# Kernel optimization log

Measured on AMD Instinct MI355X. Metric: run time of the kernel, lower is better.

## Reference

```python
import jax, jax.numpy as jnp
import numpy as np

EMBED_DIM = 512
KDIM = 64
VDIM = 64


def setup_inputs() -> dict:
    key = jax.random.key(0)
    kx, kq, kk, kv = jax.random.split(key, 4)
    B, S = 4, 4096
    x = jax.random.normal(kx, (B, S, EMBED_DIM), dtype=jnp.float32)
    # nn.Linear(embed_dim, out) weight has shape [out, embed_dim]
    WQ = jax.random.normal(kq, (KDIM, EMBED_DIM), dtype=jnp.float32) * (EMBED_DIM ** -0.5)
    WK = jax.random.normal(kk, (KDIM, EMBED_DIM), dtype=jnp.float32) * (EMBED_DIM ** -0.5)
    WV = jax.random.normal(kv, (VDIM, EMBED_DIM), dtype=jnp.float32) * (EMBED_DIM ** -0.5)
    return {"x": x, "WQ": WQ, "WK": WK, "WV": WV}


def reference(x, WQ, WK, WV):
    # q,k: [B,S,kdim]; v: [B,S,vdim] (self-attention: x[0] is x[-1])
    q = jnp.einsum('bse,ke->bsk', x, WQ)
    k = jnp.einsum('bse,ke->bsk', x, WK)
    v = jnp.einsum('bse,ve->bsv', x, WV)
    scale = k.shape[-1] ** -0.5
    scores = jnp.einsum('bqk,bsk->bqs', q, k) * scale  # [B,S,S]
    # dropout p=0.0 -> identity; masked branch in source is a no-op (non-in-place masked_fill discarded)
    attn = jax.nn.softmax(scores, axis=-1)
    out = jnp.einsum('bqs,bsv->bqv', attn, v)  # [B,S,vdim]
    return out
```

## Files before the change

### kernel.cpp

```cpp
#include <hip/hip_runtime.h>

#define BATCH 4
#define SEQ   4096
#define EMB   512
#define HD    64

typedef __attribute__((ext_vector_type(8))) short short8;
typedef __attribute__((ext_vector_type(4))) float floatx4;

static __device__ __forceinline__ unsigned short f2bf(float f) {
  unsigned u = __builtin_bit_cast(unsigned, f);
  u += 0x7fffu + ((u >> 16) & 1u);
  return (unsigned short)(u >> 16);
}
static __device__ __forceinline__ float bf2f(unsigned short h) {
  unsigned u = ((unsigned)h) << 16;
  return __builtin_bit_cast(float, u);
}
static __device__ __forceinline__ unsigned pack_hi16(float lo, float hi) {
#if __has_builtin(__builtin_amdgcn_perm)
  return __builtin_amdgcn_perm(__builtin_bit_cast(unsigned, hi),
                               __builtin_bit_cast(unsigned, lo), 0x07060302u);
#else
  return (__builtin_bit_cast(unsigned, lo) >> 16) |
         (__builtin_bit_cast(unsigned, hi) & 0xffff0000u);
#endif
}
static __device__ __forceinline__ unsigned pack_f16(float a, float b) {
#if __has_builtin(__builtin_amdgcn_cvt_pkrtz)
  typedef __fp16 fp16v2 __attribute__((ext_vector_type(2)));
  fp16v2 h = __builtin_amdgcn_cvt_pkrtz(a, b);
  return __builtin_bit_cast(unsigned, h);
#else
  _Float16 ha = (_Float16)a, hb = (_Float16)b;
  return (unsigned)__builtin_bit_cast(unsigned short, ha) |
         ((unsigned)__builtin_bit_cast(unsigned short, hb) << 16);
#endif
}
static __device__ __forceinline__ float f16_to_f32(unsigned short bits) {
  _Float16 h = __builtin_bit_cast(_Float16, bits);
  return (float)h;
}

__global__ __launch_bounds__(256) void convw_kernel(
    const float* __restrict__ WQ, const float* __restrict__ WK,
    const float* __restrict__ WV, unsigned short* __restrict__ Wpk)
{
  int t = blockIdx.x * 256 + threadIdx.x;
  int p    = t >> 12;
  int w    = (t >> 10) & 3;
  int kc   = (t >> 6) & 15;
  int lane = t & 63;
  int lr = lane & 15, g = lane >> 4;
  const float* src = (p == 0) ? WQ : ((p == 1) ? WK : WV);
  const float4* s4 = (const float4*)(src + (16 * w + lr) * EMB + kc * 32 + 8 * g);
  float4 a = s4[0], b = s4[1];
  float vv[8] = {a.x, a.y, a.z, a.w, b.x, b.y, b.z, b.w};
  short8 o;
#pragma unroll
  for (int j = 0; j < 8; ++j) {
    unsigned short h = f2bf(vv[j]);
    o[j] = (p == 3) ? (short)f2bf(vv[j] - bf2f(h)) : (short)h;
  }
  *(short8*)(Wpk + (size_t)t * 8) = o;
}

#define XST 40

__global__ __launch_bounds__(256) void proj_kernel(
    const float* __restrict__ x,
    const unsigned short* __restrict__ Wpk,
    unsigned short* __restrict__ Qb,
    unsigned short* __restrict__ Kb,
    unsigned short* __restrict__ VTb)
{
  __shared__ __align__(16) unsigned short Xh[2][32 * XST];
  __shared__ __align__(16) unsigned short Xl[2][32 * XST];

  const int tid  = threadIdx.x;
  const int lane = tid & 63;
  const int w    = tid >> 6;
  const int lr   = lane & 15, g = lane >> 4;
  const long rowBase = (long)blockIdx.x * 32;

  floatx4 accQ[2], accK[2], accV[2];
#pragma unroll
  for (int rt = 0; rt < 2; ++rt) {
    floatx4 z = {0.f, 0.f, 0.f, 0.f};
    accQ[rt] = z; accK[rt] = z; accV[rt] = z;
  }

  const int srow = tid >> 3;
  const int sc   = 4 * (tid & 7);
  const float* xbase = x + (rowBase + srow) * EMB + sc;

  auto stage_write = [&](float4 v, int buf) {
    float vv[4] = {v.x, v.y, v.z, v.w};
    ushort4 hi, lo;
#pragma unroll
    for (int i = 0; i < 4; ++i) {
      unsigned short h = f2bf(vv[i]);
      ((unsigned short*)&hi)[i] = h;
      ((unsigned short*)&lo)[i] = f2bf(vv[i] - bf2f(h));
    }
    *(ushort4*)&Xh[buf][srow * XST + sc] = hi;
    *(ushort4*)&Xl[buf][srow * XST + sc] = lo;
  };

  float4 xv = *(const float4*)(xbase);
  stage_write(xv, 0);
  float4 xnxt = *(const float4*)(xbase + 32);

#pragma unroll 2
  for (int kc = 0; kc < 16; ++kc) {
    __syncthreads();
    const unsigned short* wb = Wpk + (size_t)(w * 16 + kc) * 512 + lane * 8;
    short8 wq  = *(const short8*)(wb);
    short8 wk  = *(const short8*)(wb + 32768);
    short8 wvh = *(const short8*)(wb + 2 * 32768);
    short8 wvl = *(const short8*)(wb + 3 * 32768);
    float4 xfut;
    if (kc + 2 < 16) xfut = *(const float4*)(xbase + (kc + 2) * 32);
    const int buf = kc & 1;
#pragma unroll
    for (int rt = 0; rt < 2; ++rt) {
      short8 xh = *(const short8*)&Xh[buf][(16 * rt + lr) * XST + 8 * g];
      short8 xl = *(const short8*)&Xl[buf][(16 * rt + lr) * XST + 8 * g];
      accQ[rt] = __builtin_amdgcn_mfma_f32_16x16x32_bf16(wq, xh, accQ[rt], 0, 0, 0);
      accK[rt] = __builtin_amdgcn_mfma_f32_16x16x32_bf16(wk, xh, accK[rt], 0, 0, 0);
      accV[rt] = __builtin_amdgcn_mfma_f32_16x16x32_bf16(xh, wvh, accV[rt], 0, 0, 0);
      accV[rt] = __builtin_amdgcn_mfma_f32_16x16x32_bf16(xl, wvh, accV[rt], 0, 0, 0);
      accV[rt] = __builtin_amdgcn_mfma_f32_16x16x32_bf16(xh, wvl, accV[rt], 0, 0, 0);
    }
    if (kc + 1 < 16) { stage_write(xnxt, (kc + 1) & 1); xnxt = xfut; }
  }

  const int bb  = (int)(rowBase >> 12);
  const int sIn = (int)(rowBase & 4095);
#pragma unroll
  for (int rt = 0; rt < 2; ++rt) {
    {
      long row = rowBase + 16 * rt + lr;
      int  col = 16 * w + 4 * g;
      ushort4 u; u.x = f2bf(accQ[rt][0]); u.y = f2bf(accQ[rt][1]);
      u.z = f2bf(accQ[rt][2]); u.w = f2bf(accQ[rt][3]);
      *(ushort4*)(Qb + row * HD + col) = u;
      ushort4 v; v.x = f2bf(accK[rt][0]); v.y = f2bf(accK[rt][1]);
      v.z = f2bf(accK[rt][2]); v.w = f2bf(accK[rt][3]);
      *(ushort4*)(Kb + row * HD + col) = v;
    }
    {
      long addr = ((long)(bb * 64 + 16 * w + lr)) * SEQ + sIn + 16 * rt + 4 * g;
      ushort4 u; u.x = f2bf(accV[rt][0]); u.y = f2bf(accV[rt][1]);
      u.z = f2bf(accV[rt][2]); u.w = f2bf(accV[rt][3]);
      *(ushort4*)(VTb + addr) = u;
    }
  }
}

#define PST 72

__global__ __launch_bounds__(256, 2) void flash_kernel(
    const unsigned short* __restrict__ Qb,
    const unsigned short* __restrict__ Kb,
    const unsigned short* __restrict__ VTb,
    unsigned short* __restrict__ Opart,
    float* __restrict__ Lpart)
{
  __shared__ __align__(16) unsigned short K0lds[64 * 64];
  __shared__ __align__(16) unsigned short V0lds[64 * 64];
  __shared__ __align__(16) unsigned short K1lds[64 * 64];
  __shared__ __align__(16) unsigned short V1lds[64 * 64];
  __shared__ __align__(16) unsigned short Plds[4][64 * PST];

  const int tid  = threadIdx.x;
  const int lane = tid & 63;
  const int w    = tid >> 6;
  const int lr   = lane & 15, g = lane >> 4;
  const int qb   = blockIdx.x >> 3;
  const int ks   = blockIdx.x & 7;
  const int bb   = qb >> 4;
  const long qrow0 = (long)qb * 256 + 64 * w;
  const int  kbase = ks * 512;

  short8 qf[4][2];
#pragma unroll
  for (int qh = 0; qh < 4; ++qh)
#pragma unroll
    for (int ec = 0; ec < 2; ++ec)
      qf[qh][ec] = *(const short8*)(Qb + (qrow0 + 16 * qh + lr) * HD + ec * 32 + 8 * g);

  floatx4 accO[4][4];
#pragma unroll
  for (int qh = 0; qh < 4; ++qh)
#pragma unroll
    for (int t = 0; t < 4; ++t) { floatx4 z = {0.f,0.f,0.f,0.f}; accO[qh][t] = z; }
  float lsum[4] = {0.f, 0.f, 0.f, 0.f};
  const float cp = 0.18033688011112042f;
  const float SH = 2.0f;

#define STAGE(kt_, KL, VL) do {                                               \
    const int k0_ = kbase + (kt_) * 64;                                       \
    _Pragma("unroll")                                                         \
    for (int h_ = 0; h_ < 2; ++h_) {                                          \
      int ci_  = h_ * 256 + tid;                                              \
      int row_ = ci_ >> 3;                                                    \
      int cc_  = (ci_ & 7) ^ (row_ & 7);                                      \
      const unsigned short* gK_ = Kb + ((long)bb * SEQ + k0_ + row_) * HD + cc_ * 8; \
      __builtin_amdgcn_global_load_lds(                                       \
          (const __attribute__((address_space(1))) void*)gK_,                 \
          (__attribute__((address_space(3))) void*)((KL) + ci_ * 8), 16, 0, 0); \
      const unsigned short* gV_ = VTb + ((long)bb * HD + row_) * SEQ + k0_ + cc_ * 8; \
      __builtin_amdgcn_global_load_lds(                                       \
          (const __attribute__((address_space(1))) void*)gV_,                 \
          (__attribute__((address_space(3))) void*)((VL) + ci_ * 8), 16, 0, 0); \
    }                                                                         \
  } while (0)

#define COMPUTE(KL, VL) do {                                                  \
    short8 kf[2][4];                                                          \
    _Pragma("unroll")                                                         \
    for (int ec = 0; ec < 2; ++ec)                                            \
      _Pragma("unroll")                                                       \
      for (int t = 0; t < 4; ++t) {                                           \
        int key  = 16 * t + lr;                                               \
        int slot = key * 8 + ((4 * ec + g) ^ (key & 7));                      \
        kf[ec][t] = *(const short8*)((KL) + slot * 8);                        \
      }                                                                       \
    _Pragma("unroll")                                                         \
    for (int qh = 0; qh < 4; ++qh) {                                          \
      floatx4 s_[4];                                                          \
      _Pragma("unroll")                                                       \
      for (int t = 0; t < 4; ++t) { floatx4 z = {0.f,0.f,0.f,0.f}; s_[t] = z; } \
      _Pragma("unroll")                                                       \
      for (int ec = 0; ec < 2; ++ec)                                          \
        _Pragma("unroll")                                                     \
        for (int t = 0; t < 4; ++t)                                           \
          s_[t] = __builtin_amdgcn_mfma_f32_16x16x32_bf16(kf[ec][t], qf[qh][ec], s_[t], 0, 0, 0); \
      unsigned short* prow = &Plds[w][(16 * qh + lr) * PST];                  \
      float ls = 0.0f;                                                        \
      _Pragma("unroll")                                                       \
      for (int t = 0; t < 4; ++t) {                                           \
        float p0 = __builtin_amdgcn_exp2f(__builtin_fmaf(s_[t][0], cp, -SH)); \
        float p1 = __builtin_amdgcn_exp2f(__builtin_fmaf(s_[t][1], cp, -SH)); \
        float p2 = __builtin_amdgcn_exp2f(__builtin_fmaf(s_[t][2], cp, -SH)); \
        float p3 = __builtin_amdgcn_exp2f(__builtin_fmaf(s_[t][3], cp, -SH)); \
        uint2 u;                                                              \
        u.x = pack_hi16(p0, p1);                                              \
        u.y = pack_hi16(p2, p3);                                              \
        ls += __builtin_bit_cast(float, u.x << 16);                           \
        ls += __builtin_bit_cast(float, u.x & 0xffff0000u);                   \
        ls += __builtin_bit_cast(float, u.y << 16);                           \
        ls += __builtin_bit_cast(float, u.y & 0xffff0000u);                   \
        *(uint2*)(prow + 16 * t + 4 * g) = u;                                 \
      }                                                                       \
      lsum[qh] += ls;                                                         \
    }                                                                         \
    short8 vf[2][4];                                                          \
    _Pragma("unroll")                                                         \
    for (int c = 0; c < 2; ++c)                                               \
      _Pragma("unroll")                                                       \
      for (int t = 0; t < 4; ++t) {                                           \
        int d    = 16 * t + lr;                                               \
        int slot = d * 8 + ((4 * c + g) ^ (d & 7));                           \
        vf[c][t] = *(const short8*)((VL) + slot * 8);                         \
      }                                                                       \
    _Pragma("unroll")                                                         \
    for (int qh = 0; qh < 4; ++qh)                                            \
      _Pragma("unroll")                                                       \
      for (int c = 0; c < 2; ++c) {                                           \
        short8 pf = *(const short8*)(&Plds[w][(16 * qh + lr) * PST + 32 * c + 8 * g]); \
        _Pragma("unroll")                                                     \
        for (int t = 0; t < 4; ++t)                                           \
          accO[qh][t] = __builtin_amdgcn_mfma_f32_16x16x32_bf16(vf[c][t], pf, accO[qh][t], 0, 0, 0); \
      }                                                                       \
  } while (0)

  STAGE(0, K0lds, V0lds);
  for (int kt = 0; kt < 8; kt += 2) {
    __syncthreads();
    STAGE(kt + 1, K1lds, V1lds);
    COMPUTE(K0lds, V0lds);
    __syncthreads();
    if (kt + 2 < 8) STAGE(kt + 2, K0lds, V0lds);
    COMPUTE(K1lds, V1lds);
  }
#undef STAGE
#undef COMPUTE

  unsigned short* obase = Opart + (size_t)(qb * 8 + ks) * 256 * HD;
#pragma unroll
  for (int qh = 0; qh < 4; ++qh) {
    float l = lsum[qh];
    l += __shfl_xor(l, 16, 64);
    l += __shfl_xor(l, 32, 64);
    int qlocal = 64 * w + 16 * qh + lr;
#pragma unroll
    for (int t = 0; t < 4; ++t) {
      uint2 u;
      u.x = pack_f16(accO[qh][t][0], accO[qh][t][1]);
      u.y = pack_f16(accO[qh][t][2], accO[qh][t][3]);
      *(uint2*)(obase + qlocal * HD + 16 * t + 4 * g) = u;
    }
    if (g == 0) Lpart[(qb * 8 + ks) * 256 + qlocal] = l;
  }
}

__global__ __launch_bounds__(256) void combine_kernel(
    const unsigned short* __restrict__ Opart, const float* __restrict__ Lpart,
    float* __restrict__ out)
{
  int t   = blockIdx.x * 256 + threadIdx.x;
  int row = t >> 4;
  int d0  = (t & 15) * 4;
  int qb = row >> 8, qi = row & 255;
  float4 acc = {0.f, 0.f, 0.f, 0.f};
  float lt = 0.0f;
#pragma unroll
  for (int ks = 0; ks < 8; ++ks) {
    const unsigned short* p = Opart + ((size_t)(qb * 8 + ks) * 256 + qi) * HD + d0;
    ushort4 v = *(const ushort4*)p;
    acc.x += f16_to_f32(v.x);
    acc.y += f16_to_f32(v.y);
    acc.z += f16_to_f32(v.z);
    acc.w += f16_to_f32(v.w);
    lt += Lpart[(qb * 8 + ks) * 256 + qi];
  }
  float inv = 1.0f / lt;
  float4 o = {acc.x * inv, acc.y * inv, acc.z * inv, acc.w * inv};
  *(float4*)(out + (size_t)row * HD + d0) = o;
}

extern "C" void kernel_launch(void* const* d_in, const int* in_sizes, int n_in,
                              void* d_out, int out_size, void* d_ws, size_t ws_size,
                              hipStream_t stream) {
  const float* x  = (const float*)d_in[0];
  const float* WQ = (const float*)d_in[1];
  const float* WK = (const float*)d_in[2];
  const float* WV = (const float*)d_in[3];

  unsigned short* Qb  = (unsigned short*)d_ws;
  unsigned short* Kb  = Qb  + (size_t)BATCH * SEQ * HD;
  unsigned short* VTb = Kb  + (size_t)BATCH * SEQ * HD;
  unsigned short* Wpk = VTb + (size_t)BATCH * SEQ * HD;
  unsigned short* Opart = Wpk + 262144;
  float* Lpart = (float*)(Opart + (size_t)512 * 256 * HD);

  convw_kernel<<<64, 256, 0, stream>>>(WQ, WK, WV, Wpk);
  proj_kernel<<<(BATCH * SEQ) / 32, 256, 0, stream>>>(x, Wpk, Qb, Kb, VTb);
  flash_kernel<<<512, 256, 0, stream>>>(Qb, Kb, VTb, Opart, Lpart);
  combine_kernel<<<1024, 256, 0, stream>>>(Opart, Lpart, (float*)d_out);
}
```

Baseline: 119.6 us.

## Prefetch weights and x deeper, compute row sums via MFMA, add setprio

The projection kernel now double-buffers the packed weight fragments in registers and prefetches x four chunks ahead, issuing those loads before the barrier so global latency overlaps the MFMA work. The attention kernel drops the per-element VALU row-sum accumulation and its cross-lane shuffles, and instead computes the softmax denominator with an extra MFMA against a vector of bf16 ones. It also wraps the MFMA blocks in s_setprio to favour issuing matrix ops. In exchange, register pressure rises and the attention kernel does about 12% more MFMA work.

```diff
diff --git a/kernel.cpp b/kernel.cpp
--- a/kernel.cpp
+++ b/kernel.cpp
@@ -107,32 +107,45 @@
     *(ushort4*)&Xl[buf][srow * XST + sc] = lo;
   };
 
+  short8 Wb[2][4];
+  {
+    const unsigned short* wb_ = Wpk + (size_t)(w * 16) * 512 + lane * 8;
+    Wb[0][0] = *(const short8*)(wb_);
+    Wb[0][1] = *(const short8*)(wb_ + 32768);
+    Wb[0][2] = *(const short8*)(wb_ + 2 * 32768);
+    Wb[0][3] = *(const short8*)(wb_ + 3 * 32768);
+  }
+
   float4 xv = *(const float4*)(xbase);
   stage_write(xv, 0);
-  float4 xnxt = *(const float4*)(xbase + 32);
+  float4 xn1 = *(const float4*)(xbase + 32);
+  float4 xn2 = *(const float4*)(xbase + 64);
+  float4 xn3 = *(const float4*)(xbase + 96);
 
 #pragma unroll 2
   for (int kc = 0; kc < 16; ++kc) {
+    if (kc + 1 < 16) {
+      const unsigned short* wb_ = Wpk + (size_t)(w * 16 + kc + 1) * 512 + lane * 8;
+      Wb[(kc + 1) & 1][0] = *(const short8*)(wb_);
+      Wb[(kc + 1) & 1][1] = *(const short8*)(wb_ + 32768);
+      Wb[(kc + 1) & 1][2] = *(const short8*)(wb_ + 2 * 32768);
+      Wb[(kc + 1) & 1][3] = *(const short8*)(wb_ + 3 * 32768);
+    }
+    float4 xfut;
+    if (kc + 4 < 16) xfut = *(const float4*)(xbase + (kc + 4) * 32);
     __syncthreads();
-    const unsigned short* wb = Wpk + (size_t)(w * 16 + kc) * 512 + lane * 8;
-    short8 wq  = *(const short8*)(wb);
-    short8 wk  = *(const short8*)(wb + 32768);
-    short8 wvh = *(const short8*)(wb + 2 * 32768);
-    short8 wvl = *(const short8*)(wb + 3 * 32768);
-    float4 xfut;
-    if (kc + 2 < 16) xfut = *(const float4*)(xbase + (kc + 2) * 32);
     const int buf = kc & 1;
 #pragma unroll
     for (int rt = 0; rt < 2; ++rt) {
       short8 xh = *(const short8*)&Xh[buf][(16 * rt + lr) * XST + 8 * g];
       short8 xl = *(const short8*)&Xl[buf][(16 * rt + lr) * XST + 8 * g];
-      accQ[rt] = __builtin_amdgcn_mfma_f32_16x16x32_bf16(wq, xh, accQ[rt], 0, 0, 0);
-      accK[rt] = __builtin_amdgcn_mfma_f32_16x16x32_bf16(wk, xh, accK[rt], 0, 0, 0);
-      accV[rt] = __builtin_amdgcn_mfma_f32_16x16x32_bf16(xh, wvh, accV[rt], 0, 0, 0);
-      accV[rt] = __builtin_amdgcn_mfma_f32_16x16x32_bf16(xl, wvh, accV[rt], 0, 0, 0);
-      accV[rt] = __builtin_amdgcn_mfma_f32_16x16x32_bf16(xh, wvl, accV[rt], 0, 0, 0);
-    }
-    if (kc + 1 < 16) { stage_write(xnxt, (kc + 1) & 1); xnxt = xfut; }
+      accQ[rt] = __builtin_amdgcn_mfma_f32_16x16x32_bf16(Wb[buf][0], xh, accQ[rt], 0, 0, 0);
+      accK[rt] = __builtin_amdgcn_mfma_f32_16x16x32_bf16(Wb[buf][1], xh, accK[rt], 0, 0, 0);
+      accV[rt] = __builtin_amdgcn_mfma_f32_16x16x32_bf16(xh, Wb[buf][2], accV[rt], 0, 0, 0);
+      accV[rt] = __builtin_amdgcn_mfma_f32_16x16x32_bf16(xl, Wb[buf][2], accV[rt], 0, 0, 0);
+      accV[rt] = __builtin_amdgcn_mfma_f32_16x16x32_bf16(xh, Wb[buf][3], accV[rt], 0, 0, 0);
+    }
+    if (kc + 1 < 16) { stage_write(xn1, (kc + 1) & 1); xn1 = xn2; xn2 = xn3; xn3 = xfut; }
   }
 
   const int bb  = (int)(rowBase >> 12);
@@ -191,11 +204,18 @@
       qf[qh][ec] = *(const short8*)(Qb + (qrow0 + 16 * qh + lr) * HD + ec * 32 + 8 * g);
 
   floatx4 accO[4][4];
-#pragma unroll
-  for (int qh = 0; qh < 4; ++qh)
-#pragma unroll
-    for (int t = 0; t < 4; ++t) { floatx4 z = {0.f,0.f,0.f,0.f}; accO[qh][t] = z; }
-  float lsum[4] = {0.f, 0.f, 0.f, 0.f};
+  floatx4 accL[4];
+#pragma unroll
+  for (int qh = 0; qh < 4; ++qh) {
+    floatx4 z = {0.f, 0.f, 0.f, 0.f};
+#pragma unroll
+    for (int t = 0; t < 4; ++t) accO[qh][t] = z;
+    accL[qh] = z;
+  }
+  short8 onesf;
+#pragma unroll
+  for (int j = 0; j < 8; ++j) onesf[j] = (short)0x3F80;
+
   const float cp = 0.18033688011112042f;
   const float SH = 2.0f;
 
@@ -232,13 +252,14 @@
       floatx4 s_[4];                                                          \
       _Pragma("unroll")                                                       \
       for (int t = 0; t < 4; ++t) { floatx4 z = {0.f,0.f,0.f,0.f}; s_[t] = z; } \
+      __builtin_amdgcn_s_setprio(1);                                          \
       _Pragma("unroll")                                                       \
       for (int ec = 0; ec < 2; ++ec)                                          \
         _Pragma("unroll")                                                     \
         for (int t = 0; t < 4; ++t)                                           \
           s_[t] = __builtin_amdgcn_mfma_f32_16x16x32_bf16(kf[ec][t], qf[qh][ec], s_[t], 0, 0, 0); \
+      __builtin_amdgcn_s_setprio(0);                                          \
       unsigned short* prow = &Plds[w][(16 * qh + lr) * PST];                  \
-      float ls = 0.0f;                                                        \
       _Pragma("unroll")                                                       \
       for (int t = 0; t < 4; ++t) {                                           \
         float p0 = __builtin_amdgcn_exp2f(__builtin_fmaf(s_[t][0], cp, -SH)); \
@@ -248,13 +269,8 @@
         uint2 u;                                                              \
         u.x = pack_hi16(p0, p1);                                              \
         u.y = pack_hi16(p2, p3);                                              \
-        ls += __builtin_bit_cast(float, u.x << 16);                           \
-        ls += __builtin_bit_cast(float, u.x & 0xffff0000u);                   \
-        ls += __builtin_bit_cast(float, u.y << 16);                           \
-        ls += __builtin_bit_cast(float, u.y & 0xffff0000u);                   \
         *(uint2*)(prow + 16 * t + 4 * g) = u;                                 \
       }                                                                       \
-      lsum[qh] += ls;                                                         \
     }                                                                         \
     short8 vf[2][4];                                                          \
     _Pragma("unroll")                                                         \
@@ -270,9 +286,12 @@
       _Pragma("unroll")                                                       \
       for (int c = 0; c < 2; ++c) {                                           \
         short8 pf = *(const short8*)(&Plds[w][(16 * qh + lr) * PST + 32 * c + 8 * g]); \
+        __builtin_amdgcn_s_setprio(1);                                        \
         _Pragma("unroll")                                                     \
         for (int t = 0; t < 4; ++t)                                           \
           accO[qh][t] = __builtin_amdgcn_mfma_f32_16x16x32_bf16(vf[c][t], pf, accO[qh][t], 0, 0, 0); \
+        accL[qh] = __builtin_amdgcn_mfma_f32_16x16x32_bf16(onesf, pf, accL[qh], 0, 0, 0); \
+        __builtin_amdgcn_s_setprio(0);                                        \
       }                                                                       \
   } while (0)
 
@@ -291,9 +310,6 @@
   unsigned short* obase = Opart + (size_t)(qb * 8 + ks) * 256 * HD;
 #pragma unroll
   for (int qh = 0; qh < 4; ++qh) {
-    float l = lsum[qh];
-    l += __shfl_xor(l, 16, 64);
-    l += __shfl_xor(l, 32, 64);
     int qlocal = 64 * w + 16 * qh + lr;
 #pragma unroll
     for (int t = 0; t < 4; ++t) {
@@ -302,7 +318,7 @@
       u.y = pack_f16(accO[qh][t][2], accO[qh][t][3]);
       *(uint2*)(obase + qlocal * HD + 16 * t + 4 * g) = u;
     }
-    if (g == 0) Lpart[(qb * 8 + ks) * 256 + qlocal] = l;
+    if (g == 0) Lpart[(qb * 8 + ks) * 256 + qlocal] = accL[qh][0];
   }
 }
 
```

After: 120.0 us. No clear change (+0.4%).
